# Kernel tuning notes

Measured on AMD Instinct MI355X. Metric: run time of the kernel, lower is better.

## Reference

```python
import jax, jax.numpy as jnp
import numpy as np

B, T, F, U = 64, 512, 1024, 256


def setup_inputs() -> dict:
    key = jax.random.key(0)
    ks = jax.random.split(key, 9)
    x = jax.random.normal(ks[0], (B, T, F), dtype=jnp.float32)
    # variable-length sequences, zero-padded tail (Masking layer semantics)
    lengths = jax.random.randint(ks[1], (B,), T // 2, T + 1)
    valid = (jnp.arange(T)[None, :] < lengths[:, None]).astype(jnp.float32)
    x = x * valid[:, :, None]
    s_fc = 1.0 / np.sqrt(F)
    s_u = 1.0 / np.sqrt(U)
    W_fc = jax.random.uniform(ks[2], (F, U), jnp.float32, -s_fc, s_fc)
    b_fc = jnp.zeros((U,), jnp.float32)
    W_x = jax.random.uniform(ks[3], (U, 4 * U), jnp.float32, -s_u, s_u)
    W_h = jax.random.uniform(ks[4], (U, 4 * U), jnp.float32, -s_u, s_u)
    # Keras unit_forget_bias: ones for forget-gate slice, zeros elsewhere
    b_lstm = jnp.concatenate([jnp.zeros((U,)), jnp.ones((U,)), jnp.zeros((2 * U,))]).astype(jnp.float32)
    W_p = jax.random.uniform(ks[5], (U, 1), jnp.float32, -s_u, s_u)
    b_p = jnp.zeros((1,), jnp.float32)
    return {"inputs": x, "W_fc": W_fc, "b_fc": b_fc, "W_x": W_x,
            "W_h": W_h, "b_lstm": b_lstm, "W_p": W_p, "b_p": b_p}


def _forward(inputs, W_fc, b_fc, W_x, W_h, b_lstm, W_p, b_p):
    # Masking layer: timestep masked iff ALL features == 0.0
    mask = jnp.any(inputs != 0.0, axis=-1)              # [B, T] bool
    x = inputs * mask[:, :, None].astype(inputs.dtype)  # Masking zeroes masked steps
    # Dense(units, relu) applied per timestep
    z = jax.nn.relu(jnp.einsum('btf,fu->btu', x, W_fc) + b_fc)  # [B, T, U]

    units = W_h.shape[0]
    h0 = jnp.zeros((x.shape[0], units), x.dtype)
    c0 = jnp.zeros((x.shape[0], units), x.dtype)

    def step(carry, xt_mt):
        h, c = carry
        xt, mt = xt_mt                                   # [B, U], [B]
        gates = xt @ W_x + h @ W_h + b_lstm              # [B, 4U]
        i, f, g, o = jnp.split(gates, 4, axis=-1)
        i = jax.nn.sigmoid(i)
        f = jax.nn.sigmoid(f)
        g = jnp.tanh(g)
        o = jax.nn.sigmoid(o)
        c_new = f * c + i * g
        h_new = o * jnp.tanh(c_new)
        m = mt[:, None]
        # Keras masked-RNN semantics: skip step, carry previous h/c and output
        h2 = jnp.where(m, h_new, h)
        c2 = jnp.where(m, c_new, c)
        return (h2, c2), h2

    z_t = jnp.swapaxes(z, 0, 1)        # [T, B, U]
    m_t = jnp.swapaxes(mask, 0, 1)     # [T, B]
    _, hs = jax.lax.scan(step, (h0, c0), (z_t, m_t))
    hs = jnp.swapaxes(hs, 0, 1)        # [B, T, U]
    # Dense(1, sigmoid) prediction head
    return jax.nn.sigmoid(jnp.einsum('btu,uo->bto', hs, W_p) + b_p)  # [B, T, 1]


def reference(inputs, W_fc, b_fc, W_x, W_h, b_lstm, W_p, b_p):
    return _forward(inputs, W_fc, b_fc, W_x, W_h, b_lstm, W_p, b_p)
```

## Files before the change

kernel.cpp:

```cpp
#include <hip/hip_runtime.h>
#include <hip/hip_fp16.h>
#include <hip/hip_fp8.h>
#include <cstdint>

#define BB 64
#define TT 512
#define FF 1024
#define UU 256
#define GG 1024

typedef _Float16 f16x8 __attribute__((ext_vector_type(8)));
typedef float f32x4 __attribute__((ext_vector_type(4)));
typedef int i32x8 __attribute__((ext_vector_type(8)));

typedef union { uint4 u4[2]; i32x8 v; } pk32;

__device__ __forceinline__ float sigmf_(float x) { return 1.f / (1.f + __expf(-x)); }
__device__ __forceinline__ float tanhf_(float x) { return 1.f - 2.f / (1.f + __expf(2.f * x)); }

__global__ __launch_bounds__(256) void mask_kernel(const float* __restrict__ x,
                                                   float* __restrict__ maskF) {
  int row = blockIdx.x;
  int tid = threadIdx.x;
  const float4* xr = (const float4*)(x + (size_t)row * FF);
  float4 v = xr[tid];
  bool nz = (v.x != 0.f) || (v.y != 0.f) || (v.z != 0.f) || (v.w != 0.f);
  __shared__ int flag;
  if (tid == 0) flag = 0;
  __syncthreads();
  if (__any(nz)) {
    if ((tid & 63) == 0) atomicOr(&flag, 1);
  }
  __syncthreads();
  if (tid == 0) maskF[row] = flag ? 1.f : 0.f;
}

__global__ __launch_bounds__(256) void pack_whP(const float* __restrict__ Wh,
                                                uint8_t* __restrict__ whP) {
  int col = blockIdx.x;
  int k = threadIdx.x;
  __hip_fp8_e4m3 f(Wh[(size_t)k * GG + col] * 16.f);
  whP[col * 256 + k] = (uint8_t)f.__x;
}

template <typename TA, bool RELU>
__global__ __launch_bounds__(256) void gemm16(const TA* __restrict__ A,
                                              const float* __restrict__ Bm,
                                              const float* __restrict__ bias,
                                              __half* __restrict__ C,
                                              int M, int N, int K) {
  __shared__ _Float16 As[128][40];
  __shared__ _Float16 Bs[64][40];
  int tid = threadIdx.x;
  int lane = tid & 63, w = tid >> 6;
  int wm = w & 1, wn = w >> 1;
  int m0 = blockIdx.x * 128, n0 = blockIdx.y * 64;
  int fr = lane & 15, ks = lane >> 4;

  f32x4 acc[4][2];
#pragma unroll
  for (int i = 0; i < 4; ++i)
#pragma unroll
    for (int j = 0; j < 2; ++j) acc[i][j] = (f32x4){0.f, 0.f, 0.f, 0.f};

  for (int k0 = 0; k0 < K; k0 += 32) {
    {
      int r = tid >> 3, kq = (tid & 7) * 4;
#pragma unroll
      for (int i = 0; i < 4; ++i) {
        int row = r + 32 * i;
        const TA* src = A + (size_t)(m0 + row) * K + k0 + kq;
        if constexpr (sizeof(TA) == 4) {
          float4 v = *reinterpret_cast<const float4*>(src);
          union { uint2 u; _Float16 h[4]; } pk;
          pk.h[0] = (_Float16)v.x; pk.h[1] = (_Float16)v.y;
          pk.h[2] = (_Float16)v.z; pk.h[3] = (_Float16)v.w;
          *reinterpret_cast<uint2*>(&As[row][kq]) = pk.u;
        } else {
          uint2 v = *reinterpret_cast<const uint2*>(src);
          *reinterpret_cast<uint2*>(&As[row][kq]) = v;
        }
      }
      int nn = tid & 63, kb = tid >> 6;
#pragma unroll
      for (int i = 0; i < 8; ++i) {
        int kk = kb + 4 * i;
        Bs[nn][kk] = (_Float16)Bm[(size_t)(k0 + kk) * N + n0 + nn];
      }
    }
    __syncthreads();
    f16x8 af[4], bf[2];
#pragma unroll
    for (int fm = 0; fm < 4; ++fm)
      af[fm] = *reinterpret_cast<const f16x8*>(&As[wm * 64 + fm * 16 + fr][ks * 8]);
#pragma unroll
    for (int fn = 0; fn < 2; ++fn)
      bf[fn] = *reinterpret_cast<const f16x8*>(&Bs[wn * 32 + fn * 16 + fr][ks * 8]);
#pragma unroll
    for (int fm = 0; fm < 4; ++fm)
#pragma unroll
      for (int fn = 0; fn < 2; ++fn)
        acc[fm][fn] = __builtin_amdgcn_mfma_f32_16x16x32_f16(af[fm], bf[fn], acc[fm][fn], 0, 0, 0);
    __syncthreads();
  }
#pragma unroll
  for (int fm = 0; fm < 4; ++fm)
#pragma unroll
    for (int fn = 0; fn < 2; ++fn) {
      int mg0 = m0 + wm * 64 + fm * 16 + ks * 4;
      int ng = n0 + wn * 32 + fn * 16 + fr;
      float bv = bias[ng];
#pragma unroll
      for (int r = 0; r < 4; ++r) {
        float v = acc[fm][fn][r] + bv;
        if constexpr (RELU) v = fmaxf(v, 0.f);
        C[(size_t)(mg0 + r) * N + ng] = __float2half(v);
      }
    }
}

__attribute__((amdgpu_waves_per_eu(4, 4)))
__global__ void __launch_bounds__(1024, 1)
lstm_rec(const uint8_t* __restrict__ whP,
         const __half* __restrict__ zxh,
         const float* __restrict__ maskF,
         const float* __restrict__ Wp,
         __half* __restrict__ ppG)
{
  __shared__ __align__(16) uint8_t hpk[2][256];

  const int b = blockIdx.x;
  const int t = threadIdx.x;
  const int lane = t & 63, w = t >> 6;
  const int fr = lane & 15, q = lane >> 4;
  const int SC1 = 0x7F7F7F7F;

  const uint4* whP4 = (const uint4*)whP;

  pk32 bfr[2][4];
#pragma unroll
  for (int kt = 0; kt < 2; ++kt)
#pragma unroll
    for (int ct = 0; ct < 4; ++ct) {
      int col = ct * 256 + w * 16 + fr;
      bfr[kt][ct].u4[0] = whP4[col * 16 + kt * 8 + q * 2];
      bfr[kt][ct].u4[1] = whP4[col * 16 + kt * 8 + q * 2 + 1];
    }
#pragma unroll
  for (int kt = 0; kt < 2; ++kt)
#pragma unroll
    for (int ct = 0; ct < 4; ++ct) {
      asm volatile("" : "+v"(bfr[kt][ct].u4[0].x), "+v"(bfr[kt][ct].u4[0].y),
                        "+v"(bfr[kt][ct].u4[0].z), "+v"(bfr[kt][ct].u4[0].w));
      asm volatile("" : "+v"(bfr[kt][ct].u4[1].x), "+v"(bfr[kt][ct].u4[1].y),
                        "+v"(bfr[kt][ct].u4[1].z), "+v"(bfr[kt][ct].u4[1].w));
    }

  if (t < 64) ((uint32_t*)hpk[0])[t] = 0u;
  float c_state = 0.f, h_state = 0.f;
  float wpv = Wp[w * 16 + fr];
  __syncthreads();

  const __half* zp = zxh + (size_t)b * TT * GG;
  const float* mrow = maskF + b * TT;
  __half* ppp = ppG + (size_t)b * TT * UU;
  const int u = w * 16 + fr;

  __half zi_c = zp[u], zf_c = zp[u + 256], zg_c = zp[u + 512], zo_c = zp[u + 768];
  float mval_c = mrow[0];
  __half pp_prev = __float2half(0.f);

  int p = 0;
  for (int step = 0; step < TT; ++step) {
    if (step > 0 && q == 0) ppp[(size_t)(step - 1) * UU + u] = pp_prev;

    const __half* zq = zp + ((step + 1 < TT) ? GG : 0);
    int sn = (step + 1 < TT) ? step + 1 : step;
    __half zi_n = zq[u], zf_n = zq[u + 256], zg_n = zq[u + 512], zo_n = zq[u + 768];
    float mval_n = mrow[sn];

    const uint4* hp4 = (const uint4*)hpk[p];
    f32x4 d0 = {0.f, 0.f, 0.f, 0.f}, d1 = d0, d2 = d0, d3 = d0;
#pragma unroll
    for (int kt = 0; kt < 2; ++kt) {
      pk32 a;
      a.u4[0] = hp4[kt * 8 + q * 2];
      a.u4[1] = hp4[kt * 8 + q * 2 + 1];
      d0 = __builtin_amdgcn_mfma_scale_f32_16x16x128_f8f6f4(
          a.v, bfr[kt][0].v, d0, 0, 0, 0, SC1, 0, SC1);
      d1 = __builtin_amdgcn_mfma_scale_f32_16x16x128_f8f6f4(
          a.v, bfr[kt][1].v, d1, 0, 0, 0, SC1, 0, SC1);
      d2 = __builtin_amdgcn_mfma_scale_f32_16x16x128_f8f6f4(
          a.v, bfr[kt][2].v, d2, 0, 0, 0, SC1, 0, SC1);
      d3 = __builtin_amdgcn_mfma_scale_f32_16x16x128_f8f6f4(
          a.v, bfr[kt][3].v, d3, 0, 0, 0, SC1, 0, SC1);
    }

    {
      float gi = fmaf(d0[0], 0.0625f, __half2float(zi_c));
      float gf = fmaf(d1[0], 0.0625f, __half2float(zf_c));
      float gg = fmaf(d2[0], 0.0625f, __half2float(zg_c));
      float go = fmaf(d3[0], 0.0625f, __half2float(zo_c));
      float ig = sigmf_(gi);
      float fg = sigmf_(gf);
      float g_ = tanhf_(gg);
      float og = sigmf_(go);
      float cn = fg * c_state + ig * g_;
      float hn = og * tanhf_(cn);
      bool on = (mval_c > 0.5f);
      c_state = on ? cn : c_state;
      h_state = on ? hn : h_state;
      __hip_fp8_e4m3 f8(h_state);
      if (q == 0) hpk[p ^ 1][u] = (uint8_t)f8.__x;
      pp_prev = __float2half(h_state * wpv);
    }
    __syncthreads();
    p ^= 1;
    zp += GG;
    zi_c = zi_n; zf_c = zf_n; zg_c = zg_n; zo_c = zo_n; mval_c = mval_n;
  }
  if (q == 0) ppp[(size_t)(TT - 1) * UU + u] = pp_prev;
}

__global__ __launch_bounds__(256) void proj_kernel(const __half* __restrict__ ppG,
                                                   const float* __restrict__ bp,
                                                   float* __restrict__ out) {
  int row = blockIdx.x * 4 + (threadIdx.x >> 6);
  int lane = threadIdx.x & 63;
  const ushort4* pr = (const ushort4*)(ppG + (size_t)row * UU);
  ushort4 v = pr[lane];
  __half2 a = *reinterpret_cast<__half2*>(&v.x);
  __half2 c = *reinterpret_cast<__half2*>(&v.z);
  float2 af = __half22float2(a), cf = __half22float2(c);
  float s = af.x + af.y + cf.x + cf.y;
#pragma unroll
  for (int off = 32; off > 0; off >>= 1) s += __shfl_down(s, off);
  if (lane == 0) out[row] = 1.f / (1.f + __expf(-(s + bp[0])));
}

extern "C" void kernel_launch(void* const* d_in, const int* in_sizes, int n_in,
                              void* d_out, int out_size, void* d_ws, size_t ws_size,
                              hipStream_t stream) {
  const float* x = (const float*)d_in[0];
  const float* Wfc = (const float*)d_in[1];
  const float* bfc = (const float*)d_in[2];
  const float* Wx = (const float*)d_in[3];
  const float* Wh = (const float*)d_in[4];
  const float* blstm = (const float*)d_in[5];
  const float* Wp = (const float*)d_in[6];
  const float* bp = (const float*)d_in[7];
  float* out = (float*)d_out;

  char* ws = (char*)d_ws;
  float* maskF = (float*)(ws);
  __half* zh = (__half*)(ws + 131072);
  __half* zxh = (__half*)(ws + 131072 + 16777216);
  uint8_t* whP = (uint8_t*)(ws + 131072 + 16777216 + 67108864);
  __half* ppG = zh;

  mask_kernel<<<BB * TT, 256, 0, stream>>>(x, maskF);
  pack_whP<<<GG, 256, 0, stream>>>(Wh, whP);
  gemm16<float, true><<<dim3((BB * TT) / 128, UU / 64), 256, 0, stream>>>(
      x, Wfc, bfc, zh, BB * TT, UU, FF);
  gemm16<__half, false><<<dim3((BB * TT) / 128, GG / 64), 256, 0, stream>>>(
      zh, Wx, blstm, zxh, BB * TT, GG, UU);
  lstm_rec<<<BB, 1024, 0, stream>>>(whP, zxh, maskF, Wp, ppG);
  proj_kernel<<<(BB * TT) / 4, 256, 0, stream>>>(ppG, bp, out);
}
```

Before: 737.9 us.

## Interleave gate preactivations per unit, stage mask in LDS, lighten step barrier

```diff
diff --git a/kernel.cpp b/kernel.cpp
--- a/kernel.cpp
+++ b/kernel.cpp
@@ -43,7 +43,7 @@
   whP[col * 256 + k] = (uint8_t)f.__x;
 }
 
-template <typename TA, bool RELU>
+template <typename TA, bool RELU, bool PERM>
 __global__ __launch_bounds__(256) void gemm16(const TA* __restrict__ A,
                                               const float* __restrict__ Bm,
                                               const float* __restrict__ bias,
@@ -110,11 +110,12 @@
       int mg0 = m0 + wm * 64 + fm * 16 + ks * 4;
       int ng = n0 + wn * 32 + fn * 16 + fr;
       float bv = bias[ng];
+      int ngs = PERM ? ((ng & 255) * 4 + (ng >> 8)) : ng;
 #pragma unroll
       for (int r = 0; r < 4; ++r) {
         float v = acc[fm][fn][r] + bv;
         if constexpr (RELU) v = fmaxf(v, 0.f);
-        C[(size_t)(mg0 + r) * N + ng] = __float2half(v);
+        C[(size_t)(mg0 + r) * N + ngs] = __float2half(v);
       }
     }
 }
@@ -122,12 +123,13 @@
 __attribute__((amdgpu_waves_per_eu(4, 4)))
 __global__ void __launch_bounds__(1024, 1)
 lstm_rec(const uint8_t* __restrict__ whP,
-         const __half* __restrict__ zxh,
+         const __half* __restrict__ zxi,
          const float* __restrict__ maskF,
          const float* __restrict__ Wp,
          __half* __restrict__ ppG)
 {
   __shared__ __align__(16) uint8_t hpk[2][256];
+  __shared__ float mlds[TT];
 
   const int b = blockIdx.x;
   const int t = threadIdx.x;
@@ -157,27 +159,25 @@
     }
 
   if (t < 64) ((uint32_t*)hpk[0])[t] = 0u;
+  if (t < TT) mlds[t] = maskF[b * TT + t];
   float c_state = 0.f, h_state = 0.f;
   float wpv = Wp[w * 16 + fr];
   __syncthreads();
 
-  const __half* zp = zxh + (size_t)b * TT * GG;
-  const float* mrow = maskF + b * TT;
+  const uint2* zp = (const uint2*)(zxi + (size_t)b * TT * GG);
   __half* ppp = ppG + (size_t)b * TT * UU;
   const int u = w * 16 + fr;
 
-  __half zi_c = zp[u], zf_c = zp[u + 256], zg_c = zp[u + 512], zo_c = zp[u + 768];
-  float mval_c = mrow[0];
+  uint2 zx_c = zp[u];
   __half pp_prev = __float2half(0.f);
 
   int p = 0;
   for (int step = 0; step < TT; ++step) {
     if (step > 0 && q == 0) ppp[(size_t)(step - 1) * UU + u] = pp_prev;
 
-    const __half* zq = zp + ((step + 1 < TT) ? GG : 0);
-    int sn = (step + 1 < TT) ? step + 1 : step;
-    __half zi_n = zq[u], zf_n = zq[u + 256], zg_n = zq[u + 512], zo_n = zq[u + 768];
-    float mval_n = mrow[sn];
+    const uint2* zq = zp + ((step + 1 < TT) ? 256 : 0);
+    uint2 zx_n = zq[u];
+    float mval = mlds[step];
 
     const uint4* hp4 = (const uint4*)hpk[p];
     f32x4 d0 = {0.f, 0.f, 0.f, 0.f}, d1 = d0, d2 = d0, d3 = d0;
@@ -197,27 +197,33 @@
     }
 
     {
-      float gi = fmaf(d0[0], 0.0625f, __half2float(zi_c));
-      float gf = fmaf(d1[0], 0.0625f, __half2float(zf_c));
-      float gg = fmaf(d2[0], 0.0625f, __half2float(zg_c));
-      float go = fmaf(d3[0], 0.0625f, __half2float(zo_c));
+      union { uint2 u2; __half2 h2[2]; } zz;
+      zz.u2 = zx_c;
+      float2 zif = __half22float2(zz.h2[0]);
+      float2 zgo = __half22float2(zz.h2[1]);
+      float gi = fmaf(d0[0], 0.0625f, zif.x);
+      float gf = fmaf(d1[0], 0.0625f, zif.y);
+      float gg = fmaf(d2[0], 0.0625f, zgo.x);
+      float go = fmaf(d3[0], 0.0625f, zgo.y);
       float ig = sigmf_(gi);
       float fg = sigmf_(gf);
       float g_ = tanhf_(gg);
       float og = sigmf_(go);
       float cn = fg * c_state + ig * g_;
       float hn = og * tanhf_(cn);
-      bool on = (mval_c > 0.5f);
+      bool on = (mval > 0.5f);
       c_state = on ? cn : c_state;
       h_state = on ? hn : h_state;
       __hip_fp8_e4m3 f8(h_state);
       if (q == 0) hpk[p ^ 1][u] = (uint8_t)f8.__x;
       pp_prev = __float2half(h_state * wpv);
     }
-    __syncthreads();
+    asm volatile("s_waitcnt lgkmcnt(0)" ::: "memory");
+    __builtin_amdgcn_s_barrier();
+    asm volatile("" ::: "memory");
     p ^= 1;
-    zp += GG;
-    zi_c = zi_n; zf_c = zf_n; zg_c = zg_n; zo_c = zo_n; mval_c = mval_n;
+    zp += 256;
+    zx_c = zx_n;
   }
   if (q == 0) ppp[(size_t)(TT - 1) * UU + u] = pp_prev;
 }
@@ -254,16 +260,16 @@
   char* ws = (char*)d_ws;
   float* maskF = (float*)(ws);
   __half* zh = (__half*)(ws + 131072);
-  __half* zxh = (__half*)(ws + 131072 + 16777216);
+  __half* zxi = (__half*)(ws + 131072 + 16777216);
   uint8_t* whP = (uint8_t*)(ws + 131072 + 16777216 + 67108864);
   __half* ppG = zh;
 
   mask_kernel<<<BB * TT, 256, 0, stream>>>(x, maskF);
   pack_whP<<<GG, 256, 0, stream>>>(Wh, whP);
-  gemm16<float, true><<<dim3((BB * TT) / 128, UU / 64), 256, 0, stream>>>(
+  gemm16<float, true, false><<<dim3((BB * TT) / 128, UU / 64), 256, 0, stream>>>(
       x, Wfc, bfc, zh, BB * TT, UU, FF);
-  gemm16<__half, false><<<dim3((BB * TT) / 128, GG / 64), 256, 0, stream>>>(
-      zh, Wx, blstm, zxh, BB * TT, GG, UU);
-  lstm_rec<<<BB, 1024, 0, stream>>>(whP, zxh, maskF, Wp, ppG);
+  gemm16<__half, false, true><<<dim3((BB * TT) / 128, GG / 64), 256, 0, stream>>>(
+      zh, Wx, blstm, zxi, BB * TT, GG, UU);
+  lstm_rec<<<BB, 1024, 0, stream>>>(whP, zxi, maskF, Wp, ppG);
   proj_kernel<<<(BB * TT) / 4, 256, 0, stream>>>(ppG, bp, out);
 }
```

New measurement: 773.7 us. 1.05x slower.
